# Kernel tuning notes

Measured on AMD Instinct MI355X. Metric: run time of the kernel, lower is better.

Reference implementation:

```python
import jax, jax.numpy as jnp
import numpy as np

N = 400000        # pixel nodes (B images ~224x224)
E = 3200000       # edges, avg degree 8
B = 8             # images
NUM_SP = 150      # superpixels per image (<= 196, per assert)
S = B * NUM_SP    # total superpixel segments
GRID = 14 * 14    # fixed 14x14 grid = 196 slots
DIMS = [24, 8, 16, 32, 64, 64]  # conv_out_dim=24 -> channels//8 ... channels=64


def setup_inputs():
    key = jax.random.key(0)
    ks = jax.random.split(key, 16)
    inp = {}
    inp["x"] = jax.random.normal(ks[0], (N, DIMS[0]), jnp.float32)
    inp["edge_index"] = jax.random.randint(ks[1], (2, E), 0, N, jnp.int32)
    inp["batch_idx"] = jnp.sort(jax.random.randint(ks[2], (N,), 0, S, jnp.int32))
    inp["num_sp"] = jnp.full((B,), NUM_SP, jnp.int32)
    for i in range(5):
        fi, fo = DIMS[i], DIMS[i + 1]
        inp[f"W{i+1}"] = jax.random.normal(ks[3 + i], (fi, fo), jnp.float32) * (2.0 / fi) ** 0.5
        inp[f"b{i+1}"] = jnp.zeros((fo,), jnp.float32)
        inp[f"g{i+1}"] = jnp.ones((fo,), jnp.float32)
        inp[f"be{i+1}"] = jnp.zeros((fo,), jnp.float32)
    C = DIMS[-1]
    inp["Wp"] = jax.random.normal(ks[9], (4 * C, C), jnp.float32) * (2.0 / (4 * C)) ** 0.5
    inp["bp"] = jnp.zeros((C,), jnp.float32)
    return inp


def _forward(x, edge_index, batch_idx, num_sp, layers, Wp, bp):
    n = x.shape[0]
    # GCNConv: add self-loops, symmetric normalization D^-1/2 (A+I) D^-1/2
    loop = jnp.arange(n, dtype=edge_index.dtype)
    src = jnp.concatenate([edge_index[0], loop])
    dst = jnp.concatenate([edge_index[1], loop])
    deg = jax.ops.segment_sum(jnp.ones_like(dst, dtype=jnp.float32), dst, num_segments=n)
    dis = jax.lax.rsqrt(deg)  # deg >= 1 due to self-loops
    norm = dis[src] * dis[dst]  # [E+N]

    h = x
    for i, (W, b, g, be) in enumerate(layers):
        h = h @ W                                                   # [N, fo]
        h = jax.ops.segment_sum(h[src] * norm[:, None], dst, num_segments=n) + b
        # BatchNorm (training mode: batch stats over all nodes)
        mu = h.mean(axis=0)
        var = h.var(axis=0)
        h = g * (h - mu) * jax.lax.rsqrt(var + 1e-5) + be
        if i < 4:  # last BN feeds the aggregator directly (no ReLU)
            h = jax.nn.relu(h)

    # MultiAggregation(['mean','min','max','std'], mode='proj') over superpixel ids
    cnt = jnp.maximum(jax.ops.segment_sum(jnp.ones((n, 1), jnp.float32), batch_idx, num_segments=S), 1.0)
    sm = jax.ops.segment_sum(h, batch_idx, num_segments=S)
    sm2 = jax.ops.segment_sum(h * h, batch_idx, num_segments=S)
    mean = sm / cnt
    std = jnp.sqrt(jax.nn.relu(sm2 / cnt - mean * mean) + 1e-5)  # PyG StdAggregation
    mn = jax.ops.segment_min(h, batch_idx, num_segments=S)
    mx = jax.ops.segment_max(h, batch_idx, num_segments=S)
    agg = jnp.concatenate([mean, mn, mx, std], axis=1) @ Wp + bp  # [S, C]

    # padding_reshape_layer: pack per-image superpixel rows into [B, C, 14, 14]
    offs = jnp.cumsum(num_sp) - num_sp                # start row of each image
    pos = jnp.arange(GRID, dtype=num_sp.dtype)
    idx = jnp.clip(offs[:, None] + pos[None, :], 0, S - 1)  # [B, 196]
    mask = pos[None, :] < num_sp[:, None]
    feats = jnp.where(mask[..., None], agg[idx], 0.0)       # [B, 196, C]
    C = agg.shape[1]
    # torch: reshape(14,14,C) then transpose(0,2) -> y[c,j,i] = x[i,j,c]
    return feats.reshape(B, 14, 14, C).transpose(0, 3, 2, 1)


def reference(x, edge_index, batch_idx, num_sp,
              W1, b1, g1, be1, W2, b2, g2, be2, W3, b3, g3, be3,
              W4, b4, g4, be4, W5, b5, g5, be5, Wp, bp):
    layers = [(W1, b1, g1, be1), (W2, b2, g2, be2), (W3, b3, g3, be3),
              (W4, b4, g4, be4), (W5, b5, g5, be5)]
    return _forward(x, edge_index, batch_idx, num_sp, layers, Wp, bp)
```

## Files before the change

### kernel.cpp

```cpp
#include <hip/hip_runtime.h>
#include <hip/hip_fp16.h>

#define TPB 256
#define BSH 9
#define BUCK (1 << BSH)
#define NBMAX 1024
#define CAP 6144

using f16x8 = __attribute__((ext_vector_type(8))) _Float16;
using f32x4 = __attribute__((ext_vector_type(4))) float;


union H8 { uint4 u; __half2 h[4]; };
union H4 { uint2 u; __half2 h[2]; };

__device__ inline void h8_to_f(const H8 v, float4& a, float4& b) {
    float2 f0 = __half22float2(v.h[0]);
    float2 f1 = __half22float2(v.h[1]);
    float2 f2 = __half22float2(v.h[2]);
    float2 f3 = __half22float2(v.h[3]);
    a = make_float4(f0.x, f0.y, f1.x, f1.y);
    b = make_float4(f2.x, f2.y, f3.x, f3.y);
}
__device__ inline H8 f_to_h8(float4 a, float4 b) {
    H8 r;
    r.h[0] = __floats2half2_rn(a.x, a.y);
    r.h[1] = __floats2half2_rn(a.z, a.w);
    r.h[2] = __floats2half2_rn(b.x, b.y);
    r.h[3] = __floats2half2_rn(b.z, b.w);
    return r;
}
__device__ inline float4 f4z() { return make_float4(0.f, 0.f, 0.f, 0.f); }
__device__ inline float4 f4axpy(float4 a, float s, float4 c) {
    return make_float4(fmaf(a.x, s, c.x), fmaf(a.y, s, c.y), fmaf(a.z, s, c.z), fmaf(a.w, s, c.w));
}
__device__ inline float4 f4relu_aff(float4 h, float4 sc, float4 sb) {
    return make_float4(fmaxf(fmaf(h.x, sc.x, sb.x), 0.f), fmaxf(fmaf(h.y, sc.y, sb.y), 0.f),
                       fmaxf(fmaf(h.z, sc.z, sb.z), 0.f), fmaxf(fmaf(h.w, sc.w, sb.w), 0.f));
}


__global__ __launch_bounds__(256) void k_bcount(const int* __restrict__ dst, int E,
                                                int* __restrict__ bcount, int nb) {
    __shared__ int hist[NBMAX];
    for (int i = threadIdx.x; i < nb; i += 256) hist[i] = 0;
    __syncthreads();
    const int e0 = blockIdx.x * 8192;
#pragma unroll 4
    for (int k = 0; k < 32; ++k) {
        int e = e0 + k * 256 + threadIdx.x;
        if (e < E) atomicAdd(&hist[dst[e] >> BSH], 1);
    }
    __syncthreads();
    for (int i = threadIdx.x; i < nb; i += 256) {
        int h = hist[i];
        if (h) atomicAdd(&bcount[i], h);
    }
}

__global__ void k_bscan(const int* __restrict__ bcount, int* __restrict__ bbase,
                        int* __restrict__ bcur, int nb, int E, int* __restrict__ row_ptr,
                        int n) {
    if (threadIdx.x == 0 && blockIdx.x == 0) {
        int run = 0;
        for (int i = 0; i < nb; ++i) {
            bbase[i] = run;
            bcur[i] = run;
            run += bcount[i];
        }
        bbase[nb] = E;
        row_ptr[n] = E;
    }
}

__global__ __launch_bounds__(256) void k_partA(const int* __restrict__ src,
                                               const int* __restrict__ dst, int E,
                                               int* __restrict__ bcur, int* __restrict__ bin,
                                               int nb) {
    __shared__ int hist[NBMAX];
    __shared__ int base[NBMAX];
    for (int i = threadIdx.x; i < nb; i += 256) hist[i] = 0;
    __syncthreads();
    const int e0 = blockIdx.x * 8192;
#pragma unroll 4
    for (int k = 0; k < 32; ++k) {
        int e = e0 + k * 256 + threadIdx.x;
        if (e < E) atomicAdd(&hist[dst[e] >> BSH], 1);
    }
    __syncthreads();
    for (int i = threadIdx.x; i < nb; i += 256) {
        int h = hist[i];
        base[i] = h ? atomicAdd(&bcur[i], h) : 0;
        hist[i] = 0;
    }
    __syncthreads();
#pragma unroll 4
    for (int k = 0; k < 32; ++k) {
        int e = e0 + k * 256 + threadIdx.x;
        if (e < E) {
            int d = dst[e];
            int b = d >> BSH;
            int off = atomicAdd(&hist[b], 1);
            bin[base[b] + off] = ((d & (BUCK - 1)) << 19) | src[e];
        }
    }
}

__global__ __launch_bounds__(256) void k_csr_bucket(const int* __restrict__ bin,
                                                    const int* __restrict__ bbase,
                                                    int* __restrict__ row_ptr,
                                                    float* __restrict__ dis,
                                                    int* __restrict__ csr_src, int n) {
    __shared__ int ldeg[BUCK];
    __shared__ int lcur[BUCK];
    __shared__ int ts[256];
    __shared__ int stage[CAP];
    const int b = blockIdx.x;
    const int node0 = b << BSH;
    const int nodes = min(BUCK, n - node0);
    const int ebeg = bbase[b], eend = bbase[b + 1];
    const int cnt = eend - ebeg;

    for (int i = threadIdx.x; i < BUCK; i += 256) ldeg[i] = 0;
    __syncthreads();
    for (int e = ebeg + threadIdx.x; e < eend; e += 256)
        atomicAdd(&ldeg[bin[e] >> 19], 1);
    __syncthreads();

    const int b2 = threadIdx.x * 2;
    int v0 = ldeg[b2], v1 = ldeg[b2 + 1];
    ts[threadIdx.x] = v0 + v1;
    __syncthreads();
    for (int off = 1; off < 256; off <<= 1) {
        int t = (threadIdx.x >= off) ? ts[threadIdx.x - off] : 0;
        __syncthreads();
        ts[threadIdx.x] += t;
        __syncthreads();
    }
    int o0 = (threadIdx.x == 0) ? 0 : ts[threadIdx.x - 1];
    int o1 = o0 + v0;
    lcur[b2] = o0;
    lcur[b2 + 1] = o1;
    if (b2 < nodes) {
        row_ptr[node0 + b2] = ebeg + o0;
        dis[node0 + b2] = rsqrtf((float)(v0 + 1));
    }
    if (b2 + 1 < nodes) {
        row_ptr[node0 + b2 + 1] = ebeg + o1;
        dis[node0 + b2 + 1] = rsqrtf((float)(v1 + 1));
    }
    __syncthreads();

    for (int e = ebeg + threadIdx.x; e < eend; e += 256) {
        int p = bin[e];
        int pos = atomicAdd(&lcur[p >> 19], 1);
        int s = p & 0x7FFFF;
        if (pos < CAP) stage[pos] = s;
        else csr_src[ebeg + pos] = s;
    }
    __syncthreads();
    int m = cnt < CAP ? cnt : CAP;
    for (int i = threadIdx.x; i < m; i += 256) csr_src[ebeg + i] = stage[i];
}


template <int FI, int FO, bool STATS, bool IN_F32>
__global__ __launch_bounds__(TPB) void k_mm_v(const void* __restrict__ tin,
                                              const float* __restrict__ W,
                                              __half* __restrict__ z,
                                              float* __restrict__ stats, int n) {
    constexpr int GROUPS = FO / 8;
    constexpr int NPB = (TPB / GROUPS) * 4;
    __shared__ float sW[FI * FO];
    __shared__ float sred[STATS ? TPB * 16 : 1];
    for (int i = threadIdx.x; i < FI * FO; i += TPB) sW[i] = W[i];
    __syncthreads();

    const int g = threadIdx.x % GROUPS;
    const int nl = threadIdx.x / GROUPS;
    const int nbase = blockIdx.x * NPB + nl * 4;

    float4 acc0[4], acc1[4];
#pragma unroll
    for (int j = 0; j < 4; ++j) { acc0[j] = f4z(); acc1[j] = f4z(); }

    for (int k = 0; k < FI; k += 4) {
        float4 wv0[4], wv1[4];
#pragma unroll
        for (int kk = 0; kk < 4; ++kk) {
            wv0[kk] = *(const float4*)&sW[(k + kk) * FO + g * 8];
            wv1[kk] = *(const float4*)&sW[(k + kk) * FO + g * 8 + 4];
        }
#pragma unroll
        for (int j = 0; j < 4; ++j) {
            int node = nbase + j;
            float rk[4] = {0.f, 0.f, 0.f, 0.f};
            if (node < n) {
                if (IN_F32) {
                    float4 rv = *(const float4*)((const float*)tin + (size_t)node * FI + k);
                    rk[0] = rv.x; rk[1] = rv.y; rk[2] = rv.z; rk[3] = rv.w;
                } else {
                    H4 hv;
                    hv.u = *(const uint2*)((const __half*)tin + (size_t)node * FI + k);
                    float2 f0 = __half22float2(hv.h[0]);
                    float2 f1 = __half22float2(hv.h[1]);
                    rk[0] = f0.x; rk[1] = f0.y; rk[2] = f1.x; rk[3] = f1.y;
                }
            }
#pragma unroll
            for (int kk = 0; kk < 4; ++kk) {
                acc0[j] = f4axpy(wv0[kk], rk[kk], acc0[j]);
                acc1[j] = f4axpy(wv1[kk], rk[kk], acc1[j]);
            }
        }
    }

#pragma unroll
    for (int j = 0; j < 4; ++j) {
        int node = nbase + j;
        if (node < n) {
            H8 o = f_to_h8(acc0[j], acc1[j]);
            *(uint4*)(z + (size_t)node * FO + g * 8) = o.u;
        }
    }

    if (STATS) {
        float4 s0 = f4z(), s1 = f4z(), q0 = f4z(), q1 = f4z();
#pragma unroll
        for (int j = 0; j < 4; ++j) {
            s0.x += acc0[j].x; s0.y += acc0[j].y; s0.z += acc0[j].z; s0.w += acc0[j].w;
            s1.x += acc1[j].x; s1.y += acc1[j].y; s1.z += acc1[j].z; s1.w += acc1[j].w;
            q0.x = fmaf(acc0[j].x, acc0[j].x, q0.x); q0.y = fmaf(acc0[j].y, acc0[j].y, q0.y);
            q0.z = fmaf(acc0[j].z, acc0[j].z, q0.z); q0.w = fmaf(acc0[j].w, acc0[j].w, q0.w);
            q1.x = fmaf(acc1[j].x, acc1[j].x, q1.x); q1.y = fmaf(acc1[j].y, acc1[j].y, q1.y);
            q1.z = fmaf(acc1[j].z, acc1[j].z, q1.z); q1.w = fmaf(acc1[j].w, acc1[j].w, q1.w);
        }
        float* slot = &sred[threadIdx.x * 16];
        *(float4*)(slot + 0) = s0;
        *(float4*)(slot + 4) = s1;
        *(float4*)(slot + 8) = q0;
        *(float4*)(slot + 12) = q1;
        __syncthreads();
        if (threadIdx.x < FO * 2) {
            int c = threadIdx.x % FO;
            int m = threadIdx.x / FO;
            int g2 = c / 8, ci = c % 8;
            float a = 0.f;
            for (int nl2 = 0; nl2 < TPB / GROUPS; ++nl2)
                a += sred[(nl2 * GROUPS + g2) * 16 + m * 8 + ci];
            atomicAdd(&stats[m * FO + c], a);
        }
    }
}


template <int FI, int ROWS>
__global__ __launch_bounds__(256) void k_gmm(const int* __restrict__ row_ptr,
                                             const int* __restrict__ csr_src,
                                             const float* __restrict__ dis,
                                             const __half* __restrict__ zin,
                                             const float* __restrict__ W,
                                             const float* __restrict__ stats_in,
                                             const float* __restrict__ gg,
                                             const float* __restrict__ be, float inv_n,
                                             __half* __restrict__ zout,
                                             float* __restrict__ stats_out, int n) {
    constexpr int RSW = FI + 8;
    constexpr int RST = FI + 8;
    constexpr int PARTS = FI / 16;
    constexpr int KC = FI / 32;
    constexpr int RT = ROWS / 64;
    constexpr int NTASK = ROWS * PARTS / 256;
    __shared__ _Float16 wt[64 * RSW];
    __shared__ _Float16 ttile[ROWS * RST];
    __shared__ float saff[2 * FI];
    __shared__ float sstat[2][4][64];

    for (int i = threadIdx.x; i < FI * 64; i += 256) {
        int k = i >> 6, nn = i & 63;
        wt[nn * RSW + k] = (_Float16)W[i];
    }
    if (threadIdx.x < FI) {
        int c = threadIdx.x;
        float mu = stats_in[c] * inv_n;
        float var = stats_in[FI + c] * inv_n - mu * mu;
        float s = gg[c] * rsqrtf(var + 1e-5f);
        saff[c] = s;
        saff[FI + c] = fmaf(-mu, s, be[c]);
    }
    __syncthreads();

    const int nbase = blockIdx.x * ROWS;

#pragma unroll
    for (int it = 0; it < NTASK; ++it) {
        int tt = it * 256 + threadIdx.x;
        int nl = tt / PARTS;
        int part = tt % PARTS;
        int node = nbase + nl;
        int cbase = part * 16;
        float4 sc[4], sb[4];
#pragma unroll
        for (int v = 0; v < 4; ++v) {
            sc[v] = *(const float4*)&saff[cbase + v * 4];
            sb[v] = *(const float4*)&saff[FI + cbase + v * 4];
        }
        float4 acc[4] = {f4z(), f4z(), f4z(), f4z()};
        if (node < n) {
            float dn = dis[node];
            float w0 = dn * dn;
            {
                const uint4* zp = (const uint4*)(zin + (size_t)node * FI + cbase);
#pragma unroll
                for (int l = 0; l < 2; ++l) {
                    H8 hv; hv.u = zp[l];
                    float4 a, b;
                    h8_to_f(hv, a, b);
                    a = f4relu_aff(a, sc[2 * l], sb[2 * l]);
                    b = f4relu_aff(b, sc[2 * l + 1], sb[2 * l + 1]);
                    acc[2 * l] = f4axpy(a, w0, acc[2 * l]);
                    acc[2 * l + 1] = f4axpy(b, w0, acc[2 * l + 1]);
                }
            }
            int beg = row_ptr[node], end = row_ptr[node + 1];
            int j = beg;
            for (; j + 1 < end; j += 2) {
                int s0 = csr_src[j], s1 = csr_src[j + 1];
                float wA = dn * dis[s0];
                float wB = dn * dis[s1];
                const uint4* pA = (const uint4*)(zin + (size_t)s0 * FI + cbase);
                const uint4* pB = (const uint4*)(zin + (size_t)s1 * FI + cbase);
                uint4 rA0 = pA[0], rA1 = pA[1], rB0 = pB[0], rB1 = pB[1];
                H8 hv; float4 a, b;
                hv.u = rA0; h8_to_f(hv, a, b);
                a = f4relu_aff(a, sc[0], sb[0]); b = f4relu_aff(b, sc[1], sb[1]);
                acc[0] = f4axpy(a, wA, acc[0]); acc[1] = f4axpy(b, wA, acc[1]);
                hv.u = rA1; h8_to_f(hv, a, b);
                a = f4relu_aff(a, sc[2], sb[2]); b = f4relu_aff(b, sc[3], sb[3]);
                acc[2] = f4axpy(a, wA, acc[2]); acc[3] = f4axpy(b, wA, acc[3]);
                hv.u = rB0; h8_to_f(hv, a, b);
                a = f4relu_aff(a, sc[0], sb[0]); b = f4relu_aff(b, sc[1], sb[1]);
                acc[0] = f4axpy(a, wB, acc[0]); acc[1] = f4axpy(b, wB, acc[1]);
                hv.u = rB1; h8_to_f(hv, a, b);
                a = f4relu_aff(a, sc[2], sb[2]); b = f4relu_aff(b, sc[3], sb[3]);
                acc[2] = f4axpy(a, wB, acc[2]); acc[3] = f4axpy(b, wB, acc[3]);
            }
            if (j < end) {
                int s0 = csr_src[j];
                float wA = dn * dis[s0];
                const uint4* pA = (const uint4*)(zin + (size_t)s0 * FI + cbase);
#pragma unroll
                for (int l = 0; l < 2; ++l) {
                    H8 hv; hv.u = pA[l];
                    float4 a, b;
                    h8_to_f(hv, a, b);
                    a = f4relu_aff(a, sc[2 * l], sb[2 * l]);
                    b = f4relu_aff(b, sc[2 * l + 1], sb[2 * l + 1]);
                    acc[2 * l] = f4axpy(a, wA, acc[2 * l]);
                    acc[2 * l + 1] = f4axpy(b, wA, acc[2 * l + 1]);
                }
            }
        }
        _Float16* tp = &ttile[nl * RST + cbase];
        *(uint4*)(tp) = f_to_h8(acc[0], acc[1]).u;
        *(uint4*)(tp + 8) = f_to_h8(acc[2], acc[3]).u;
    }
    __syncthreads();

    const int lane = threadIdx.x & 63;
    const int wv = threadIdx.x >> 6;
    const int quad = lane >> 4;
    const int mcol = lane & 15;

    f16x8 bf[4][KC];
#pragma unroll
    for (int t = 0; t < 4; ++t)
#pragma unroll
        for (int c = 0; c < KC; ++c)
            bf[t][c] = *(const f16x8*)&wt[(t * 16 + mcol) * RSW + c * 32 + quad * 8];

    float s[4] = {0.f, 0.f, 0.f, 0.f}, q[4] = {0.f, 0.f, 0.f, 0.f};

#pragma unroll
    for (int rt = 0; rt < RT; ++rt) {
        const int lrow0 = wv * RT * 16 + rt * 16;
        f16x8 a[KC];
#pragma unroll
        for (int c = 0; c < KC; ++c)
            a[c] = *(const f16x8*)&ttile[(lrow0 + mcol) * RST + c * 32 + quad * 8];
        f32x4 acc[4];
#pragma unroll
        for (int t = 0; t < 4; ++t) acc[t] = f32x4{0.f, 0.f, 0.f, 0.f};
#pragma unroll
        for (int t = 0; t < 4; ++t)
#pragma unroll
            for (int c = 0; c < KC; ++c)
                acc[t] = __builtin_amdgcn_mfma_f32_16x16x32_f16(a[c], bf[t][c], acc[t], 0, 0, 0);

#pragma unroll
        for (int t = 0; t < 4; ++t)
#pragma unroll
            for (int r = 0; r < 4; ++r) {
                int row = nbase + lrow0 + quad * 4 + r;
                if (row < n) zout[(size_t)row * 64 + t * 16 + mcol] = __float2half(acc[t][r]);
            }
#pragma unroll
        for (int t = 0; t < 4; ++t) {
            s[t] += acc[t][0] + acc[t][1] + acc[t][2] + acc[t][3];
            q[t] += acc[t][0] * acc[t][0] + acc[t][1] * acc[t][1] + acc[t][2] * acc[t][2] +
                    acc[t][3] * acc[t][3];
        }
    }

#pragma unroll
    for (int off = 16; off < 64; off <<= 1) {
#pragma unroll
        for (int t = 0; t < 4; ++t) {
            s[t] += __shfl_xor(s[t], off, 64);
            q[t] += __shfl_xor(q[t], off, 64);
        }
    }
    if (lane < 16) {
#pragma unroll
        for (int t = 0; t < 4; ++t) {
            sstat[0][wv][t * 16 + lane] = s[t];
            sstat[1][wv][t * 16 + lane] = q[t];
        }
    }
    __syncthreads();
    if (threadIdx.x < 128) {
        int c = threadIdx.x & 63, m = threadIdx.x >> 6;
        float a4 = sstat[m][0][c] + sstat[m][1][c] + sstat[m][2][c] + sstat[m][3][c];
        atomicAdd(&stats_out[m * 64 + c], a4);
    }
}


template <int F, bool AFFINE, bool STATS>
__global__ __launch_bounds__(TPB) void k_gather(const int* __restrict__ row_ptr,
                                                const int* __restrict__ csr_src,
                                                const float* __restrict__ dis,
                                                const __half* __restrict__ z,
                                                __half* __restrict__ t,
                                                const float* __restrict__ stats_in,
                                                const float* __restrict__ gg,
                                                const float* __restrict__ be, float inv_n,
                                                float* __restrict__ stats_out, int n) {
    constexpr int GW = (F < 16) ? F : 16;
    constexpr int PARTS = F / GW;
    constexpr int NV = GW / 4;
    constexpr int NL = GW / 8;
    __shared__ float sred[STATS ? TPB * 16 : 1];
    int tid = blockIdx.x * blockDim.x + threadIdx.x;
    int node = tid / PARTS;
    int part = tid % PARTS;
    bool active = node < n;
    if (!STATS && !active) return;
    const int cbase = part * GW;

    float4 sc[NV], sb[NV];
    if (AFFINE) {
#pragma unroll
        for (int v = 0; v < NV; ++v) {
            float scv[4], sbv[4];
#pragma unroll
            for (int u = 0; u < 4; ++u) {
                int c = cbase + v * 4 + u;
                float mu = stats_in[c] * inv_n;
                float var = stats_in[F + c] * inv_n - mu * mu;
                float s = gg[c] * rsqrtf(var + 1e-5f);
                scv[u] = s;
                sbv[u] = fmaf(-mu, s, be[c]);
            }
            sc[v] = make_float4(scv[0], scv[1], scv[2], scv[3]);
            sb[v] = make_float4(sbv[0], sbv[1], sbv[2], sbv[3]);
        }
    }

    float4 acc[NV];
#pragma unroll
    for (int v = 0; v < NV; ++v) acc[v] = f4z();

    if (active) {
        float dn = dis[node];
        float w0 = dn * dn;
        {
            const uint4* zp = (const uint4*)(z + (size_t)node * F + cbase);
#pragma unroll
            for (int l = 0; l < NL; ++l) {
                H8 hv; hv.u = zp[l];
                float4 a, b;
                h8_to_f(hv, a, b);
                if (AFFINE) { a = f4relu_aff(a, sc[2 * l], sb[2 * l]); b = f4relu_aff(b, sc[2 * l + 1], sb[2 * l + 1]); }
                acc[2 * l] = f4axpy(a, w0, acc[2 * l]);
                acc[2 * l + 1] = f4axpy(b, w0, acc[2 * l + 1]);
            }
        }
        int beg = row_ptr[node], end = row_ptr[node + 1];
        int j = beg;
        for (; j + 3 < end; j += 4) {
            int s0 = csr_src[j], s1 = csr_src[j + 1], s2 = csr_src[j + 2], s3 = csr_src[j + 3];
            float wA = dn * dis[s0];
            float wB = dn * dis[s1];
            float wC = dn * dis[s2];
            float wD = dn * dis[s3];
            const uint4* pA = (const uint4*)(z + (size_t)s0 * F + cbase);
            const uint4* pB = (const uint4*)(z + (size_t)s1 * F + cbase);
            const uint4* pC = (const uint4*)(z + (size_t)s2 * F + cbase);
            const uint4* pD = (const uint4*)(z + (size_t)s3 * F + cbase);
            uint4 rA[NL], rB[NL], rC[NL], rD[NL];
#pragma unroll
            for (int l = 0; l < NL; ++l) { rA[l] = pA[l]; rB[l] = pB[l]; rC[l] = pC[l]; rD[l] = pD[l]; }
#pragma unroll
            for (int l = 0; l < NL; ++l) {
                H8 hv; float4 a, b;
                hv.u = rA[l]; h8_to_f(hv, a, b);
                if (AFFINE) { a = f4relu_aff(a, sc[2 * l], sb[2 * l]); b = f4relu_aff(b, sc[2 * l + 1], sb[2 * l + 1]); }
                acc[2 * l] = f4axpy(a, wA, acc[2 * l]); acc[2 * l + 1] = f4axpy(b, wA, acc[2 * l + 1]);
                hv.u = rB[l]; h8_to_f(hv, a, b);
                if (AFFINE) { a = f4relu_aff(a, sc[2 * l], sb[2 * l]); b = f4relu_aff(b, sc[2 * l + 1], sb[2 * l + 1]); }
                acc[2 * l] = f4axpy(a, wB, acc[2 * l]); acc[2 * l + 1] = f4axpy(b, wB, acc[2 * l + 1]);
                hv.u = rC[l]; h8_to_f(hv, a, b);
                if (AFFINE) { a = f4relu_aff(a, sc[2 * l], sb[2 * l]); b = f4relu_aff(b, sc[2 * l + 1], sb[2 * l + 1]); }
                acc[2 * l] = f4axpy(a, wC, acc[2 * l]); acc[2 * l + 1] = f4axpy(b, wC, acc[2 * l + 1]);
                hv.u = rD[l]; h8_to_f(hv, a, b);
                if (AFFINE) { a = f4relu_aff(a, sc[2 * l], sb[2 * l]); b = f4relu_aff(b, sc[2 * l + 1], sb[2 * l + 1]); }
                acc[2 * l] = f4axpy(a, wD, acc[2 * l]); acc[2 * l + 1] = f4axpy(b, wD, acc[2 * l + 1]);
            }
        }
        for (; j < end; ++j) {
            int s0 = csr_src[j];
            float wA = dn * dis[s0];
            const uint4* pA = (const uint4*)(z + (size_t)s0 * F + cbase);
#pragma unroll
            for (int l = 0; l < NL; ++l) {
                H8 hv; hv.u = pA[l];
                float4 a, b;
                h8_to_f(hv, a, b);
                if (AFFINE) { a = f4relu_aff(a, sc[2 * l], sb[2 * l]); b = f4relu_aff(b, sc[2 * l + 1], sb[2 * l + 1]); }
                acc[2 * l] = f4axpy(a, wA, acc[2 * l]);
                acc[2 * l + 1] = f4axpy(b, wA, acc[2 * l + 1]);
            }
        }
        uint4* tp = (uint4*)(t + (size_t)node * F + cbase);
#pragma unroll
        for (int l = 0; l < NL; ++l) tp[l] = f_to_h8(acc[2 * l], acc[2 * l + 1]).u;
    }

    if (STATS) {
        float* slot = &sred[threadIdx.x * 16];
        *(float4*)(slot + 0) = acc[0];
        *(float4*)(slot + 4) = acc[1];
        float4 q0 = make_float4(acc[0].x * acc[0].x, acc[0].y * acc[0].y, acc[0].z * acc[0].z,
                                acc[0].w * acc[0].w);
        float4 q1 = make_float4(acc[1].x * acc[1].x, acc[1].y * acc[1].y, acc[1].z * acc[1].z,
                                acc[1].w * acc[1].w);
        *(float4*)(slot + 8) = q0;
        *(float4*)(slot + 12) = q1;
        __syncthreads();
        if (threadIdx.x < 16) {
            int c = threadIdx.x % 8;
            int m = threadIdx.x / 8;
            float a = 0.f;
            for (int t2 = 0; t2 < TPB; ++t2) a += sred[t2 * 16 + m * 8 + c];
            atomicAdd(&stats_out[m * 8 + c], a);
        }
    }
}


__device__ inline int bsearch_seg(const int* __restrict__ bidx, int n, int s) {
    int lo = 0, hi = n;
    while (lo < hi) {
        int mid = (lo + hi) >> 1;
        if (bidx[mid] < s) lo = mid + 1; else hi = mid;
    }
    return lo;
}

__global__ __launch_bounds__(TPB) void k_seg_reduce(const __half* __restrict__ z,
                                                    const int* __restrict__ bidx, int n,
                                                    float* __restrict__ aggin,
                                                    const float* __restrict__ stats,
                                                    const float* __restrict__ gg,
                                                    const float* __restrict__ be, float inv_n) {
    __shared__ int sbounds[2];
    int s = blockIdx.x;
    if (threadIdx.x < 2) sbounds[threadIdx.x] = bsearch_seg(bidx, n, s + threadIdx.x);
    __syncthreads();
    int start = sbounds[0], end = sbounds[1];
    int c = threadIdx.x & 63;
    float mu = stats[c] * inv_n;
    float var = stats[64 + c] * inv_n - mu * mu;
    float scv = gg[c] * rsqrtf(var + 1e-5f);
    float sbv = fmaf(-mu, scv, be[c]);
    int r0 = start + (threadIdx.x >> 6);
    float sm = 0.f, sm2 = 0.f, mn = INFINITY, mx = -INFINITY;
    for (int r = r0; r < end; r += 4) {
        float v = fmaf(__half2float(z[(size_t)r * 64 + c]), scv, sbv);
        sm += v;
        sm2 = fmaf(v, v, sm2);
        mn = fminf(mn, v);
        mx = fmaxf(mx, v);
    }
    __shared__ float s_sm[TPB], s_sm2[TPB], s_mn[TPB], s_mx[TPB];
    s_sm[threadIdx.x] = sm;
    s_sm2[threadIdx.x] = sm2;
    s_mn[threadIdx.x] = mn;
    s_mx[threadIdx.x] = mx;
    __syncthreads();
    if (threadIdx.x < 64) {
        for (int t = threadIdx.x + 64; t < TPB; t += 64) {
            sm += s_sm[t];
            sm2 += s_sm2[t];
            mn = fminf(mn, s_mn[t]);
            mx = fmaxf(mx, s_mx[t]);
        }
        int count = end - start;
        float cnt = (float)(count > 0 ? count : 1);
        float mean = sm / cnt;
        float var2 = sm2 / cnt - mean * mean;
        if (var2 < 0.f) var2 = 0.f;
        float sd = sqrtf(var2 + 1e-5f);
        if (count <= 0) { mn = 0.f; mx = 0.f; }
        aggin[s * 256 + c] = mean;
        aggin[s * 256 + 64 + c] = mn;
        aggin[s * 256 + 128 + c] = mx;
        aggin[s * 256 + 192 + c] = sd;
    }
}

__global__ __launch_bounds__(64) void k_proj(const float* __restrict__ aggin,
                                             const float* __restrict__ Wp,
                                             const float* __restrict__ bp,
                                             float* __restrict__ proj) {
    __shared__ float sA[256];
    int s = blockIdx.x;
    int j = threadIdx.x;
    for (int k = j; k < 256; k += 64) sA[k] = aggin[s * 256 + k];
    __syncthreads();
    float acc = bp[j];
#pragma unroll 8
    for (int k = 0; k < 256; ++k) acc = fmaf(sA[k], Wp[k * 64 + j], acc);
    proj[s * 64 + j] = acc;
}

__global__ void k_pack(const float* __restrict__ proj, const int* __restrict__ num_sp,
                       float* __restrict__ out, int B, int S) {
    int idx = blockIdx.x * blockDim.x + threadIdx.x;
    int total = B * 64 * 196;
    if (idx >= total) return;
    int ii = idx % 14;
    int jj = (idx / 14) % 14;
    int c = (idx / 196) % 64;
    int b = idx / (196 * 64);
    int p = ii * 14 + jj;
    int off = 0;
    for (int k = 0; k < b; ++k) off += num_sp[k];
    float v = 0.f;
    if (p < num_sp[b]) {
        int s = off + p;
        if (s > S - 1) s = S - 1;
        v = proj[s * 64 + c];
    }
    out[idx] = v;
}


extern "C" void kernel_launch(void* const* d_in, const int* in_sizes, int n_in,
                              void* d_out, int out_size, void* d_ws, size_t ws_size,
                              hipStream_t stream) {
    const float* x = (const float*)d_in[0];
    const int* ei = (const int*)d_in[1];
    const int* bidx = (const int*)d_in[2];
    const int* num_sp = (const int*)d_in[3];
    const float* Wl[5], * Gl[5], * BEl[5];
    for (int i = 0; i < 5; ++i) {
        Wl[i] = (const float*)d_in[4 + 4 * i];
        Gl[i] = (const float*)d_in[6 + 4 * i];
        BEl[i] = (const float*)d_in[7 + 4 * i];
    }
    const float* Wp = (const float*)d_in[24];
    const float* bp = (const float*)d_in[25];

    const int n = in_sizes[0] / 24;
    const int E = in_sizes[1] / 2;
    const int B = in_sizes[3];
    const int S = 1200;
    const int* src = ei;
    const int* dst = ei + E;
    const float inv_n = 1.0f / (float)n;
    const int nb = (n + BUCK - 1) >> BSH;

    char* w = (char*)d_ws;
    __half* bufZ = (__half*)w;  w += (size_t)n * 64 * 2;
    __half* bufT = (__half*)w;  w += (size_t)n * 64 * 2;
    float* dis = (float*)w;     w += (size_t)n * 4;
    int* row_ptr = (int*)w;     w += (size_t)(n + 64) * 4;
    int* csr_src = (int*)w;     w += (size_t)E * 4;
    int* bin = (int*)w;         w += (size_t)E * 4;
    int* bcount = (int*)w;      w += (size_t)(nb + 64) * 4;
    int* bbase = (int*)w;       w += (size_t)(nb + 64) * 4;
    int* bcur = (int*)w;        w += (size_t)(nb + 64) * 4;
    float* stats_all = (float*)w; w += 5 * 128 * 4;
    float* aggin = (float*)w;   w += (size_t)S * 256 * 4;
    float* proj = (float*)w;    w += (size_t)S * 64 * 4;
    float* st0 = stats_all;
    float* st1 = stats_all + 128;
    float* st2 = stats_all + 256;
    float* st3 = stats_all + 384;
    float* st4 = stats_all + 512;

    hipMemsetAsync(bcount, 0, (size_t)nb * 4, stream);
    hipMemsetAsync(stats_all, 0, 5 * 128 * 4, stream);
    k_bcount<<<(E + 8191) / 8192, 256, 0, stream>>>(dst, E, bcount, nb);
    k_bscan<<<1, 64, 0, stream>>>(bcount, bbase, bcur, nb, E, row_ptr, n);
    k_partA<<<(E + 8191) / 8192, 256, 0, stream>>>(src, dst, E, bcur, bin, nb);
    k_csr_bucket<<<nb, 256, 0, stream>>>(bin, bbase, row_ptr, dis, csr_src, n);

    k_mm_v<24, 8, false, true><<<(n + 1023) / 1024, TPB, 0, stream>>>(x, Wl[0], bufT, nullptr, n);
    k_gather<8, false, true><<<(n + TPB - 1) / TPB, TPB, 0, stream>>>(
        row_ptr, csr_src, dis, bufT, bufZ, nullptr, nullptr, nullptr, inv_n, st0, n);

    k_gather<8, true, false><<<(n + TPB - 1) / TPB, TPB, 0, stream>>>(
        row_ptr, csr_src, dis, bufZ, bufT, st0, Gl[0], BEl[0], inv_n, nullptr, n);
    k_mm_v<8, 16, true, false><<<(n + 511) / 512, TPB, 0, stream>>>(bufT, Wl[1], bufZ, st1, n);

    k_gather<16, true, false><<<(n + TPB - 1) / TPB, TPB, 0, stream>>>(
        row_ptr, csr_src, dis, bufZ, bufT, st1, Gl[1], BEl[1], inv_n, nullptr, n);
    k_mm_v<16, 32, true, false><<<(n + 255) / 256, TPB, 0, stream>>>(bufT, Wl[2], bufZ, st2, n);

    k_gmm<32, 256><<<(n + 255) / 256, 256, 0, stream>>>(
        row_ptr, csr_src, dis, bufZ, Wl[3], st2, Gl[2], BEl[2], inv_n, bufT, st3, n);
    k_gmm<64, 192><<<(n + 191) / 192, 256, 0, stream>>>(
        row_ptr, csr_src, dis, bufT, Wl[4], st3, Gl[3], BEl[3], inv_n, bufZ, st4, n);

    k_seg_reduce<<<S, TPB, 0, stream>>>(bufZ, bidx, n, aggin, st4, Gl[4], BEl[4], inv_n);
    k_proj<<<S, 64, 0, stream>>>(aggin, Wp, bp, proj);
    int total_out = B * 64 * 196;
    k_pack<<<(total_out + TPB - 1) / TPB, TPB, 0, stream>>>(proj, num_sp, (float*)d_out, B, S);
}
```

Before: 906.6 us.

## Gather neighbor aggregates directly into MFMA operand registers, dropping LDS staging

The fused gather+matmul kernel now has each lane aggregate neighbor features for exactly the node row and channel slice it will supply as the MFMA A-operand. The result is converted to fp16 in registers and fed straight to the matrix cores. This removes the shared-memory tile, its writes and reads, and a block barrier between the gather and GEMM phases. The 64-channel layer also changes from 192 to 256 rows per block, and the per-lane load width and node-to-lane mapping change, which may shift memory coalescing and load balance within each wave.

```diff
diff --git a/kernel.cpp b/kernel.cpp
--- a/kernel.cpp
+++ b/kernel.cpp
@@ -11,7 +11,7 @@
 using f32x4 = __attribute__((ext_vector_type(4))) float;
 
 
-union H8 { uint4 u; __half2 h[4]; };
+union H8 { uint4 u; __half2 h[4]; f16x8 f; };
 union H4 { uint2 u; __half2 h[2]; };
 
 __device__ inline void h8_to_f(const H8 v, float4& a, float4& b) {
@@ -254,7 +254,7 @@
 }
 
 
-template <int FI, int ROWS>
+template <int FI, int RT>
 __global__ __launch_bounds__(256) void k_gmm(const int* __restrict__ row_ptr,
                                              const int* __restrict__ csr_src,
                                              const float* __restrict__ dis,
@@ -265,14 +265,10 @@
                                              const float* __restrict__ be, float inv_n,
                                              __half* __restrict__ zout,
                                              float* __restrict__ stats_out, int n) {
+    constexpr int KC = FI / 32;
     constexpr int RSW = FI + 8;
-    constexpr int RST = FI + 8;
-    constexpr int PARTS = FI / 16;
-    constexpr int KC = FI / 32;
-    constexpr int RT = ROWS / 64;
-    constexpr int NTASK = ROWS * PARTS / 256;
+    constexpr int ROWS = 4 * RT * 16;
     __shared__ _Float16 wt[64 * RSW];
-    __shared__ _Float16 ttile[ROWS * RST];
     __shared__ float saff[2 * FI];
     __shared__ float sstat[2][4][64];
 
@@ -284,43 +280,56 @@
         int c = threadIdx.x;
         float mu = stats_in[c] * inv_n;
         float var = stats_in[FI + c] * inv_n - mu * mu;
-        float s = gg[c] * rsqrtf(var + 1e-5f);
-        saff[c] = s;
-        saff[FI + c] = fmaf(-mu, s, be[c]);
-    }
-    __syncthreads();
-
-    const int nbase = blockIdx.x * ROWS;
-
-#pragma unroll
-    for (int it = 0; it < NTASK; ++it) {
-        int tt = it * 256 + threadIdx.x;
-        int nl = tt / PARTS;
-        int part = tt % PARTS;
-        int node = nbase + nl;
-        int cbase = part * 16;
-        float4 sc[4], sb[4];
-#pragma unroll
-        for (int v = 0; v < 4; ++v) {
-            sc[v] = *(const float4*)&saff[cbase + v * 4];
-            sb[v] = *(const float4*)&saff[FI + cbase + v * 4];
-        }
-        float4 acc[4] = {f4z(), f4z(), f4z(), f4z()};
+        float sv = gg[c] * rsqrtf(var + 1e-5f);
+        saff[c] = sv;
+        saff[FI + c] = fmaf(-mu, sv, be[c]);
+    }
+    __syncthreads();
+
+    const int lane = threadIdx.x & 63;
+    const int wv = threadIdx.x >> 6;
+    const int quad = lane >> 4;
+    const int mcol = lane & 15;
+
+    f16x8 bf[4][KC];
+#pragma unroll
+    for (int t = 0; t < 4; ++t)
+#pragma unroll
+        for (int c = 0; c < KC; ++c)
+            bf[t][c] = *(const f16x8*)&wt[(t * 16 + mcol) * RSW + c * 32 + quad * 8];
+
+    float4 sc[2 * KC], sb[2 * KC];
+#pragma unroll
+    for (int c = 0; c < KC; ++c) {
+        sc[2 * c] = *(const float4*)&saff[c * 32 + quad * 8];
+        sc[2 * c + 1] = *(const float4*)&saff[c * 32 + quad * 8 + 4];
+        sb[2 * c] = *(const float4*)&saff[FI + c * 32 + quad * 8];
+        sb[2 * c + 1] = *(const float4*)&saff[FI + c * 32 + quad * 8 + 4];
+    }
+
+    float s[4] = {0.f, 0.f, 0.f, 0.f}, q[4] = {0.f, 0.f, 0.f, 0.f};
+
+#pragma unroll
+    for (int rt = 0; rt < RT; ++rt) {
+        const int row0 = blockIdx.x * ROWS + wv * (RT * 16) + rt * 16;
+        const int node = row0 + mcol;
+        float4 acc[2 * KC];
+#pragma unroll
+        for (int v = 0; v < 2 * KC; ++v) acc[v] = f4z();
+
         if (node < n) {
             float dn = dis[node];
             float w0 = dn * dn;
-            {
-                const uint4* zp = (const uint4*)(zin + (size_t)node * FI + cbase);
-#pragma unroll
-                for (int l = 0; l < 2; ++l) {
-                    H8 hv; hv.u = zp[l];
-                    float4 a, b;
-                    h8_to_f(hv, a, b);
-                    a = f4relu_aff(a, sc[2 * l], sb[2 * l]);
-                    b = f4relu_aff(b, sc[2 * l + 1], sb[2 * l + 1]);
-                    acc[2 * l] = f4axpy(a, w0, acc[2 * l]);
-                    acc[2 * l + 1] = f4axpy(b, w0, acc[2 * l + 1]);
-                }
+#pragma unroll
+            for (int c = 0; c < KC; ++c) {
+                H8 hv;
+                hv.u = *(const uint4*)(zin + (size_t)node * FI + c * 32 + quad * 8);
+                float4 a, b;
+                h8_to_f(hv, a, b);
+                a = f4relu_aff(a, sc[2 * c], sb[2 * c]);
+                b = f4relu_aff(b, sc[2 * c + 1], sb[2 * c + 1]);
+                acc[2 * c] = f4axpy(a, w0, acc[2 * c]);
+                acc[2 * c + 1] = f4axpy(b, w0, acc[2 * c + 1]);
             }
             int beg = row_ptr[node], end = row_ptr[node + 1];
             int j = beg;
@@ -328,87 +337,73 @@
                 int s0 = csr_src[j], s1 = csr_src[j + 1];
                 float wA = dn * dis[s0];
                 float wB = dn * dis[s1];
-                const uint4* pA = (const uint4*)(zin + (size_t)s0 * FI + cbase);
-                const uint4* pB = (const uint4*)(zin + (size_t)s1 * FI + cbase);
-                uint4 rA0 = pA[0], rA1 = pA[1], rB0 = pB[0], rB1 = pB[1];
-                H8 hv; float4 a, b;
-                hv.u = rA0; h8_to_f(hv, a, b);
-                a = f4relu_aff(a, sc[0], sb[0]); b = f4relu_aff(b, sc[1], sb[1]);
-                acc[0] = f4axpy(a, wA, acc[0]); acc[1] = f4axpy(b, wA, acc[1]);
-                hv.u = rA1; h8_to_f(hv, a, b);
-                a = f4relu_aff(a, sc[2], sb[2]); b = f4relu_aff(b, sc[3], sb[3]);
-                acc[2] = f4axpy(a, wA, acc[2]); acc[3] = f4axpy(b, wA, acc[3]);
-                hv.u = rB0; h8_to_f(hv, a, b);
-                a = f4relu_aff(a, sc[0], sb[0]); b = f4relu_aff(b, sc[1], sb[1]);
-                acc[0] = f4axpy(a, wB, acc[0]); acc[1] = f4axpy(b, wB, acc[1]);
-                hv.u = rB1; h8_to_f(hv, a, b);
-                a = f4relu_aff(a, sc[2], sb[2]); b = f4relu_aff(b, sc[3], sb[3]);
-                acc[2] = f4axpy(a, wB, acc[2]); acc[3] = f4axpy(b, wB, acc[3]);
+                uint4 rA[KC], rB[KC];
+#pragma unroll
+                for (int c = 0; c < KC; ++c) {
+                    rA[c] = *(const uint4*)(zin + (size_t)s0 * FI + c * 32 + quad * 8);
+                    rB[c] = *(const uint4*)(zin + (size_t)s1 * FI + c * 32 + quad * 8);
+                }
+#pragma unroll
+                for (int c = 0; c < KC; ++c) {
+                    H8 hv; float4 a, b;
+                    hv.u = rA[c];
+                    h8_to_f(hv, a, b);
+                    a = f4relu_aff(a, sc[2 * c], sb[2 * c]);
+                    b = f4relu_aff(b, sc[2 * c + 1], sb[2 * c + 1]);
+                    acc[2 * c] = f4axpy(a, wA, acc[2 * c]);
+                    acc[2 * c + 1] = f4axpy(b, wA, acc[2 * c + 1]);
+                    hv.u = rB[c];
+                    h8_to_f(hv, a, b);
+                    a = f4relu_aff(a, sc[2 * c], sb[2 * c]);
+                    b = f4relu_aff(b, sc[2 * c + 1], sb[2 * c + 1]);
+                    acc[2 * c] = f4axpy(a, wB, acc[2 * c]);
+                    acc[2 * c + 1] = f4axpy(b, wB, acc[2 * c + 1]);
+                }
             }
             if (j < end) {
                 int s0 = csr_src[j];
                 float wA = dn * dis[s0];
-                const uint4* pA = (const uint4*)(zin + (size_t)s0 * FI + cbase);
-#pragma unroll
-                for (int l = 0; l < 2; ++l) {
-                    H8 hv; hv.u = pA[l];
+#pragma unroll
+                for (int c = 0; c < KC; ++c) {
+                    H8 hv;
+                    hv.u = *(const uint4*)(zin + (size_t)s0 * FI + c * 32 + quad * 8);
                     float4 a, b;
                     h8_to_f(hv, a, b);
-                    a = f4relu_aff(a, sc[2 * l], sb[2 * l]);
-                    b = f4relu_aff(b, sc[2 * l + 1], sb[2 * l + 1]);
-                    acc[2 * l] = f4axpy(a, wA, acc[2 * l]);
-                    acc[2 * l + 1] = f4axpy(b, wA, acc[2 * l + 1]);
+                    a = f4relu_aff(a, sc[2 * c], sb[2 * c]);
+                    b = f4relu_aff(b, sc[2 * c + 1], sb[2 * c + 1]);
+                    acc[2 * c] = f4axpy(a, wA, acc[2 * c]);
+                    acc[2 * c + 1] = f4axpy(b, wA, acc[2 * c + 1]);
                 }
             }
         }
-        _Float16* tp = &ttile[nl * RST + cbase];
-        *(uint4*)(tp) = f_to_h8(acc[0], acc[1]).u;
-        *(uint4*)(tp + 8) = f_to_h8(acc[2], acc[3]).u;
-    }
-    __syncthreads();
-
-    const int lane = threadIdx.x & 63;
-    const int wv = threadIdx.x >> 6;
-    const int quad = lane >> 4;
-    const int mcol = lane & 15;
-
-    f16x8 bf[4][KC];
-#pragma unroll
-    for (int t = 0; t < 4; ++t)
-#pragma unroll
-        for (int c = 0; c < KC; ++c)
-            bf[t][c] = *(const f16x8*)&wt[(t * 16 + mcol) * RSW + c * 32 + quad * 8];
-
-    float s[4] = {0.f, 0.f, 0.f, 0.f}, q[4] = {0.f, 0.f, 0.f, 0.f};
-
-#pragma unroll
-    for (int rt = 0; rt < RT; ++rt) {
-        const int lrow0 = wv * RT * 16 + rt * 16;
+
         f16x8 a[KC];
 #pragma unroll
-        for (int c = 0; c < KC; ++c)
-            a[c] = *(const f16x8*)&ttile[(lrow0 + mcol) * RST + c * 32 + quad * 8];
-        f32x4 acc[4];
-#pragma unroll
-        for (int t = 0; t < 4; ++t) acc[t] = f32x4{0.f, 0.f, 0.f, 0.f};
+        for (int c = 0; c < KC; ++c) {
+            H8 cv = f_to_h8(acc[2 * c], acc[2 * c + 1]);
+            a[c] = cv.f;
+        }
+        f32x4 cacc[4];
+#pragma unroll
+        for (int t = 0; t < 4; ++t) cacc[t] = f32x4{0.f, 0.f, 0.f, 0.f};
 #pragma unroll
         for (int t = 0; t < 4; ++t)
 #pragma unroll
             for (int c = 0; c < KC; ++c)
-                acc[t] = __builtin_amdgcn_mfma_f32_16x16x32_f16(a[c], bf[t][c], acc[t], 0, 0, 0);
+                cacc[t] = __builtin_amdgcn_mfma_f32_16x16x32_f16(a[c], bf[t][c], cacc[t], 0, 0, 0);
 
 #pragma unroll
         for (int t = 0; t < 4; ++t)
 #pragma unroll
             for (int r = 0; r < 4; ++r) {
-                int row = nbase + lrow0 + quad * 4 + r;
-                if (row < n) zout[(size_t)row * 64 + t * 16 + mcol] = __float2half(acc[t][r]);
+                int row = row0 + quad * 4 + r;
+                if (row < n) zout[(size_t)row * 64 + t * 16 + mcol] = __float2half(cacc[t][r]);
             }
 #pragma unroll
         for (int t = 0; t < 4; ++t) {
-            s[t] += acc[t][0] + acc[t][1] + acc[t][2] + acc[t][3];
-            q[t] += acc[t][0] * acc[t][0] + acc[t][1] * acc[t][1] + acc[t][2] * acc[t][2] +
-                    acc[t][3] * acc[t][3];
+            s[t] += cacc[t][0] + cacc[t][1] + cacc[t][2] + cacc[t][3];
+            q[t] += cacc[t][0] * cacc[t][0] + cacc[t][1] * cacc[t][1] + cacc[t][2] * cacc[t][2] +
+                    cacc[t][3] * cacc[t][3];
         }
     }
 
@@ -730,9 +725,9 @@
         row_ptr, csr_src, dis, bufZ, bufT, st1, Gl[1], BEl[1], inv_n, nullptr, n);
     k_mm_v<16, 32, true, false><<<(n + 255) / 256, TPB, 0, stream>>>(bufT, Wl[2], bufZ, st2, n);
 
-    k_gmm<32, 256><<<(n + 255) / 256, 256, 0, stream>>>(
+    k_gmm<32, 4><<<(n + 255) / 256, 256, 0, stream>>>(
         row_ptr, csr_src, dis, bufZ, Wl[3], st2, Gl[2], BEl[2], inv_n, bufT, st3, n);
-    k_gmm<64, 192><<<(n + 191) / 192, 256, 0, stream>>>(
+    k_gmm<64, 4><<<(n + 255) / 256, 256, 0, stream>>>(
         row_ptr, csr_src, dis, bufT, Wl[4], st3, Gl[3], BEl[3], inv_n, bufZ, st4, n);
 
     k_seg_reduce<<<S, TPB, 0, stream>>>(bufZ, bidx, n, aggin, st4, Gl[4], BEl[4], inv_n);
```

New measurement: 967.7 us. +6.7%, slower.

## Split last layer into gather then MFMA matmul with fused BN stats

Applied to the files above, without the earlier changes.

Replaces the fused gather-plus-matmul kernel for the final 64-to-64 layer with two kernels. A standalone gather launched with four threads per node applies the previous BN and ReLU and aggregates neighbours. A new matmul kernel then uses 16x16x32 fp16 MFMA instructions and accumulates the column sum and sum of squares for BatchNorm. This trades an extra round trip of the intermediate fp16 activations through memory for matrix-core throughput and better gather parallelism.

```diff
diff --git a/kernel.cpp b/kernel.cpp
--- a/kernel.cpp
+++ b/kernel.cpp
@@ -11,7 +11,7 @@
 using f32x4 = __attribute__((ext_vector_type(4))) float;
 
 
-union H8 { uint4 u; __half2 h[4]; };
+union H8 { uint4 u; __half2 h[4]; f16x8 f; };
 union H4 { uint2 u; __half2 h[2]; };
 
 __device__ inline void h8_to_f(const H8 v, float4& a, float4& b) {
@@ -250,6 +250,97 @@
                 a += sred[(nl2 * GROUPS + g2) * 16 + m * 8 + ci];
             atomicAdd(&stats[m * FO + c], a);
         }
+    }
+}
+
+
+template <int FI>
+__global__ __launch_bounds__(256) void k_mm_mfma(const __half* __restrict__ tin,
+                                                 const float* __restrict__ W,
+                                                 __half* __restrict__ z,
+                                                 float* __restrict__ stats, int n) {
+    constexpr int KC = FI / 32;
+    constexpr int RSW = FI + 8;
+    __shared__ _Float16 wt[64 * RSW];
+    __shared__ float sstat[2][4][64];
+    for (int i = threadIdx.x; i < FI * 64; i += 256) {
+        int k = i >> 6, nn = i & 63;
+        wt[nn * RSW + k] = (_Float16)W[i];
+    }
+    __syncthreads();
+
+    const int lane = threadIdx.x & 63;
+    const int wv = threadIdx.x >> 6;
+    const int quad = lane >> 4;
+    const int mcol = lane & 15;
+    const int rowbase = blockIdx.x * 256 + wv * 64;
+
+    f16x8 b[4][KC];
+#pragma unroll
+    for (int t = 0; t < 4; ++t)
+#pragma unroll
+        for (int c = 0; c < KC; ++c)
+            b[t][c] = *(const f16x8*)&wt[(t * 16 + mcol) * RSW + c * 32 + quad * 8];
+
+    float s[4] = {0.f, 0.f, 0.f, 0.f}, q[4] = {0.f, 0.f, 0.f, 0.f};
+
+#pragma unroll
+    for (int rt = 0; rt < 4; ++rt) {
+        const int row0 = rowbase + rt * 16;
+        const int arow = row0 + mcol;
+        f16x8 a[KC];
+#pragma unroll
+        for (int c = 0; c < KC; ++c) {
+            if (arow < n)
+                a[c] = *(const f16x8*)((const _Float16*)tin + (size_t)arow * FI + c * 32 +
+                                       quad * 8);
+            else
+                a[c] = f16x8{0, 0, 0, 0, 0, 0, 0, 0};
+        }
+        f32x4 acc[4];
+#pragma unroll
+        for (int t = 0; t < 4; ++t) acc[t] = f32x4{0.f, 0.f, 0.f, 0.f};
+#pragma unroll
+        for (int t = 0; t < 4; ++t)
+#pragma unroll
+            for (int c = 0; c < KC; ++c)
+                acc[t] = __builtin_amdgcn_mfma_f32_16x16x32_f16(a[c], b[t][c], acc[t], 0, 0, 0);
+
+#pragma unroll
+        for (int t = 0; t < 4; ++t)
+#pragma unroll
+            for (int r = 0; r < 4; ++r) {
+                int row = row0 + quad * 4 + r;
+                if (row < n) z[(size_t)row * 64 + t * 16 + mcol] = __float2half(acc[t][r]);
+            }
+#pragma unroll
+        for (int t = 0; t < 4; ++t) {
+            s[t] += acc[t][0] + acc[t][1] + acc[t][2] + acc[t][3];
+            q[t] += acc[t][0] * acc[t][0] + acc[t][1] * acc[t][1] + acc[t][2] * acc[t][2] +
+                    acc[t][3] * acc[t][3];
+        }
+    }
+
+#pragma unroll
+    for (int off = 16; off < 64; off <<= 1) {
+#pragma unroll
+        for (int t = 0; t < 4; ++t) {
+            s[t] += __shfl_xor(s[t], off, 64);
+            q[t] += __shfl_xor(q[t], off, 64);
+        }
+    }
+    if (lane < 16) {
+#pragma unroll
+        for (int t = 0; t < 4; ++t) {
+            sstat[0][wv][t * 16 + lane] = s[t];
+            sstat[1][wv][t * 16 + lane] = q[t];
+        }
+    }
+    __syncthreads();
+    if (threadIdx.x < 128) {
+        int c = threadIdx.x & 63, m = threadIdx.x >> 6;
+        float a4 = sstat[m][0][c] + sstat[m][1][c] + sstat[m][2][c] + sstat[m][3][c];
+        atomicAdd(&stats[m * 64 + c], a4);
     }
 }
 
@@ -732,10 +823,12 @@
 
     k_gmm<32, 256><<<(n + 255) / 256, 256, 0, stream>>>(
         row_ptr, csr_src, dis, bufZ, Wl[3], st2, Gl[2], BEl[2], inv_n, bufT, st3, n);
-    k_gmm<64, 192><<<(n + 191) / 192, 256, 0, stream>>>(
-        row_ptr, csr_src, dis, bufT, Wl[4], st3, Gl[3], BEl[3], inv_n, bufZ, st4, n);
-
-    k_seg_reduce<<<S, TPB, 0, stream>>>(bufZ, bidx, n, aggin, st4, Gl[4], BEl[4], inv_n);
+
+    k_gather<64, true, false><<<(4 * n + TPB - 1) / TPB, TPB, 0, stream>>>(
+        row_ptr, csr_src, dis, bufT, bufZ, st3, Gl[3], BEl[3], inv_n, nullptr, n);
+    k_mm_mfma<64><<<(n + 255) / 256, 256, 0, stream>>>(bufZ, Wl[4], bufT, st4, n);
+
+    k_seg_reduce<<<S, TPB, 0, stream>>>(bufT, bidx, n, aggin, st4, Gl[4], BEl[4], inv_n);
     k_proj<<<S, 64, 0, stream>>>(aggin, Wp, bp, proj);
     int total_out = B * 64 * 196;
     k_pack<<<(total_out + TPB - 1) / TPB, TPB, 0, stream>>>(proj, num_sp, (float*)d_out, B, S);
```

Result: no change. 903.0 us (-0.4%).
